# Kernel optimization log

Measured on AMD Instinct MI355X. Metric: run time of the kernel, lower is better.

## Reference

```python
import jax, jax.numpy as jnp
import numpy as np

JITTER_EPS = 0.01
TOP_K = 8


def setup_inputs() -> dict:
    key = jax.random.key(0)
    k1, k2, k3 = jax.random.split(key, 3)
    N, D, E = 16384, 4096, 64
    x = jax.random.normal(k1, (N, D), dtype=jnp.float32)
    W = jax.random.normal(k2, (D, E), dtype=jnp.float32) * (1.0 / np.sqrt(D))
    score_bias = jnp.zeros((E,), dtype=jnp.float32)
    noise = jax.random.uniform(k3, (N, D), dtype=jnp.float32)
    return {"x": x, "W": W, "score_bias": score_bias, "noise": noise}


def reference(x, W, score_bias, noise):
    E = W.shape[1]
    # jitter (training mode): x * (low + noise * (high - low))
    low = 1.0 - JITTER_EPS
    span = 2.0 * JITTER_EPS
    xj = x * (low + noise * span)
    # router logits: (N, E)
    logits = jnp.einsum("nd,de->ne", xj, W)
    scores = jax.nn.softmax(logits, axis=-1)
    # bias-corrected top-k (DeepSeek-v3 aux-loss-free balancing): indices from
    # biased scores (no grad), weights gathered from unbiased scores.
    biased = jax.lax.stop_gradient(scores) + score_bias[None, :]
    _, expert_indices = jax.lax.top_k(biased, TOP_K)  # (N, top_k) int32
    expert_weights = jnp.take_along_axis(scores, expert_indices, axis=-1)
    # L2-normalize expert weights per token
    norm = jnp.sqrt(jnp.sum(expert_weights * expert_weights, axis=-1, keepdims=True))
    expert_weights = expert_weights / norm
    # histc over expert indices -> batch size per expert
    batch_size_per_expert = jnp.bincount(expert_indices.reshape(-1), length=E)
    return (logits, scores, expert_weights, expert_indices, batch_size_per_expert)
```

## Files before the change

### kernel.cpp

```cpp
#include <hip/hip_runtime.h>
#include <math.h>


#define N_TOK 16384
#define DIM   4096
#define NEXP  64
#define TOPK  8

#define BM 64
#define BK 64
#define KSPLIT 4
#define KCHUNKS (DIM / (BK * KSPLIT))
#define XS_STRIDE 68

template<int ATOMIC_OUT>
__global__ __launch_bounds__(256, 4) void gemm_logits_kernel(
    const float* __restrict__ x, const float* __restrict__ W,
    const float* __restrict__ noise, float* __restrict__ out)
{
    __shared__ float xs[BM * XS_STRIDE];
    __shared__ float ws[BK * NEXP];

    const int t = threadIdx.x;
    const int rowBase = blockIdx.x * BM;
    const int kOff = blockIdx.y * (DIM / KSPLIT);
    const int eg = t & 15;
    const int rg = t >> 4;

    float acc[4][4];
#pragma unroll
    for (int m = 0; m < 4; ++m)
#pragma unroll
        for (int n = 0; n < 4; ++n) acc[m][n] = 0.0f;

    float4 px[4], pn[4], pw[4];

#pragma unroll
    for (int i = 0; i < 4; ++i) {
        const int f  = t + i * 256;
        const int r  = f >> 4;
        const int c4 = f & 15;
        const size_t g = (size_t)(rowBase + r) * DIM + (size_t)(kOff + c4 * 4);
        px[i] = *(const float4*)(x + g);
        pn[i] = *(const float4*)(noise + g);
        pw[i] = *(const float4*)(W + (size_t)kOff * NEXP + (size_t)f * 4);
    }

    for (int kt = 0; kt < KCHUNKS; ++kt) {
        __syncthreads();
#pragma unroll
        for (int i = 0; i < 4; ++i) {
            const int f  = t + i * 256;
            const int r  = f >> 4;
            const int c4 = f & 15;
            const float4 xv = px[i], nv = pn[i];
            float4 j;
            j.x = xv.x * (0.99f + 0.02f * nv.x);
            j.y = xv.y * (0.99f + 0.02f * nv.y);
            j.z = xv.z * (0.99f + 0.02f * nv.z);
            j.w = xv.w * (0.99f + 0.02f * nv.w);
            *(float4*)&xs[r * XS_STRIDE + c4 * 4] = j;
            *(float4*)&ws[f * 4] = pw[i];
        }
        __syncthreads();

        if (kt + 1 < KCHUNKS) {
            const int k0 = kOff + (kt + 1) * BK;
#pragma unroll
            for (int i = 0; i < 4; ++i) {
                const int f  = t + i * 256;
                const int r  = f >> 4;
                const int c4 = f & 15;
                const size_t g = (size_t)(rowBase + r) * DIM + (size_t)(k0 + c4 * 4);
                px[i] = *(const float4*)(x + g);
                pn[i] = *(const float4*)(noise + g);
                pw[i] = *(const float4*)(W + (size_t)k0 * NEXP + (size_t)f * 4);
            }
        }

        const float4* xs4 = (const float4*)xs;
        const float4* ws4 = (const float4*)ws;
#pragma unroll 4
        for (int kk4 = 0; kk4 < 16; ++kk4) {
            const float4 b0 = ws4[(kk4 * 4 + 0) * 16 + eg];
            const float4 b1 = ws4[(kk4 * 4 + 1) * 16 + eg];
            const float4 b2 = ws4[(kk4 * 4 + 2) * 16 + eg];
            const float4 b3 = ws4[(kk4 * 4 + 3) * 16 + eg];
#pragma unroll
            for (int m = 0; m < 4; ++m) {
                const float4 a = xs4[(rg * 4 + m) * 17 + kk4];
                acc[m][0] += a.x * b0.x; acc[m][1] += a.x * b0.y;
                acc[m][2] += a.x * b0.z; acc[m][3] += a.x * b0.w;
                acc[m][0] += a.y * b1.x; acc[m][1] += a.y * b1.y;
                acc[m][2] += a.y * b1.z; acc[m][3] += a.y * b1.w;
                acc[m][0] += a.z * b2.x; acc[m][1] += a.z * b2.y;
                acc[m][2] += a.z * b2.z; acc[m][3] += a.z * b2.w;
                acc[m][0] += a.w * b3.x; acc[m][1] += a.w * b3.y;
                acc[m][2] += a.w * b3.z; acc[m][3] += a.w * b3.w;
            }
        }
    }

    if (ATOMIC_OUT) {
#pragma unroll
        for (int m = 0; m < 4; ++m)
#pragma unroll
            for (int n = 0; n < 4; ++n)
                atomicAdd(out + (size_t)(rowBase + rg * 4 + m) * NEXP + eg * 4 + n,
                          acc[m][n]);
    } else {
        float* dst = out + (size_t)blockIdx.y * N_TOK * NEXP;
#pragma unroll
        for (int m = 0; m < 4; ++m) {
            float4 o;
            o.x = acc[m][0]; o.y = acc[m][1]; o.z = acc[m][2]; o.w = acc[m][3];
            *(float4*)(dst + (size_t)(rowBase + rg * 4 + m) * NEXP + eg * 4) = o;
        }
    }
}

__global__ __launch_bounds__(64, 1) void router_topk_kernel(
    const float* part, int nsplit, int writeLogits,
    const float* __restrict__ score_bias,
    float* logits, float* __restrict__ scores,
    float* __restrict__ weights, float* __restrict__ indicesF,
    float* __restrict__ histF)
{
    __shared__ float tile[64 * 65];
    __shared__ float bs[NEXP];
    __shared__ int   hist[NEXP];

    const int t = threadIdx.x;
    const int rowBase = blockIdx.x * 64;
    bs[t] = score_bias[t];
    hist[t] = 0;
    __syncthreads();

    const size_t sstride = (size_t)N_TOK * NEXP;

#pragma unroll
    for (int i = 0; i < 16; ++i) {
        const int f   = t + i * 64;
        const int row = f >> 4;
        const int c4  = f & 15;
        const size_t g = (size_t)(rowBase + row) * NEXP + (size_t)(c4 * 4);
        float4 v = *(const float4*)(part + g);
        for (int s = 1; s < nsplit; ++s) {
            const float4 p = *(const float4*)(part + (size_t)s * sstride + g);
            v.x += p.x; v.y += p.y; v.z += p.z; v.w += p.w;
        }
        if (writeLogits) *(float4*)(logits + g) = v;
        float* dst = &tile[row * 65 + c4 * 4];
        dst[0] = v.x; dst[1] = v.y; dst[2] = v.z; dst[3] = v.w;
    }
    __syncthreads();

    float a[NEXP];
#pragma unroll
    for (int j = 0; j < NEXP; ++j) a[j] = tile[t * 65 + j];

    float m0 = a[0], m1 = a[1], m2 = a[2], m3 = a[3];
#pragma unroll
    for (int j = 4; j < NEXP; j += 4) {
        m0 = fmaxf(m0, a[j + 0]); m1 = fmaxf(m1, a[j + 1]);
        m2 = fmaxf(m2, a[j + 2]); m3 = fmaxf(m3, a[j + 3]);
    }
    const float mx = fmaxf(fmaxf(m0, m1), fmaxf(m2, m3));

    float s0 = 0.f, s1 = 0.f, s2 = 0.f, s3 = 0.f;
#pragma unroll
    for (int j = 0; j < NEXP; j += 4) {
        a[j + 0] = expf(a[j + 0] - mx); s0 += a[j + 0];
        a[j + 1] = expf(a[j + 1] - mx); s1 += a[j + 1];
        a[j + 2] = expf(a[j + 2] - mx); s2 += a[j + 2];
        a[j + 3] = expf(a[j + 3] - mx); s3 += a[j + 3];
    }
    const float sinv = 1.0f / ((s0 + s1) + (s2 + s3));
#pragma unroll
    for (int j = 0; j < NEXP; ++j) a[j] *= sinv;

#pragma unroll
    for (int j = 0; j < NEXP; ++j) tile[t * 65 + j] = a[j];

#pragma unroll
    for (int j = 0; j < NEXP; ++j) a[j] += bs[j];

    float wv[TOPK]; int wi[TOPK];
    float ssq = 0.0f;
#pragma unroll
    for (int k = 0; k < TOPK; ++k) {
        float mA = a[0],  mB = a[16], mC = a[32], mD = a[48];
        int   iA = 0,     iB = 16,    iC = 32,    iD = 48;
#pragma unroll
        for (int j = 1; j < 16; ++j) {
            if (a[j]      > mA) { mA = a[j];      iA = j; }
            if (a[16 + j] > mB) { mB = a[16 + j]; iB = 16 + j; }
            if (a[32 + j] > mC) { mC = a[32 + j]; iC = 32 + j; }
            if (a[48 + j] > mD) { mD = a[48 + j]; iD = 48 + j; }
        }
        float m = mA; int mi = iA;
        if (mB > m) { m = mB; mi = iB; }
        if (mC > m) { m = mC; mi = iC; }
        if (mD > m) { m = mD; mi = iD; }

        const float w = tile[t * 65 + mi];
        wv[k] = w; wi[k] = mi; ssq += w * w;
#pragma unroll
        for (int j = 0; j < NEXP; ++j) if (j == mi) a[j] = -INFINITY;
    }

    const float rn = 1.0f / sqrtf(ssq);
    const size_t ro = (size_t)(rowBase + t) * TOPK;
#pragma unroll
    for (int k = 0; k < TOPK; ++k) {
        weights[ro + k]  = wv[k] * rn;
        indicesF[ro + k] = (float)wi[k];
        atomicAdd(&hist[wi[k]], 1);
    }
    __syncthreads();

#pragma unroll
    for (int i = 0; i < 16; ++i) {
        const int f   = t + i * 64;
        const int row = f >> 4;
        const int c4  = f & 15;
        const float* src = &tile[row * 65 + c4 * 4];
        float4 o; o.x = src[0]; o.y = src[1]; o.z = src[2]; o.w = src[3];
        *(float4*)(scores + (size_t)(rowBase + row) * NEXP + (size_t)(c4 * 4)) = o;
    }
    atomicAdd(&histF[t], (float)hist[t]);
}

extern "C" void kernel_launch(void* const* d_in, const int* in_sizes, int n_in,
                              void* d_out, int out_size, void* d_ws, size_t ws_size,
                              hipStream_t stream)
{
    const float* x     = (const float*)d_in[0];
    const float* W     = (const float*)d_in[1];
    const float* sbias = (const float*)d_in[2];
    const float* noise = (const float*)d_in[3];

    float* out      = (float*)d_out;
    float* logits   = out;
    float* scores   = out + (size_t)N_TOK * NEXP;
    float* weights  = out + 2ull * N_TOK * NEXP;
    float* indicesF = weights + (size_t)N_TOK * TOPK;
    float* histF    = indicesF + (size_t)N_TOK * TOPK;

    hipMemsetAsync(histF, 0, NEXP * sizeof(float), stream);

    const size_t partialBytes = (size_t)KSPLIT * N_TOK * NEXP * sizeof(float);
    dim3 ggrid(N_TOK / BM, KSPLIT);

    if (d_ws != nullptr && ws_size >= partialBytes) {
        float* partial = (float*)d_ws;
        gemm_logits_kernel<0><<<ggrid, 256, 0, stream>>>(x, W, noise, partial);
        router_topk_kernel<<<N_TOK / 64, 64, 0, stream>>>(
            partial, KSPLIT, 1, sbias, logits, scores, weights, indicesF, histF);
    } else {
        hipMemsetAsync(logits, 0, (size_t)N_TOK * NEXP * sizeof(float), stream);
        gemm_logits_kernel<1><<<ggrid, 256, 0, stream>>>(x, W, noise, logits);
        router_topk_kernel<<<N_TOK / 64, 64, 0, stream>>>(
            logits, 1, 0, sbias, logits, scores, weights, indicesF, histF);
    }
}
```

Before: 626.3 us.

## Double-buffer GEMM shared tiles with XOR swizzle and 2x8 thread tiles

Rewrites the jittered-logits GEMM main loop to use two shared-memory buffers with a BK of 32. This allows one barrier per chunk, with the next chunk's global loads issued before compute and staged after it. The x tile now uses an XOR swizzle instead of padding to avoid LDS bank conflicts. The per-thread tile changes from 4x4 to 2x8. These changes target barrier stalls and LDS conflicts, at the cost of more loop iterations and a changed register and LDS access pattern.

After: 580.9 us. -7.3%, faster.

```diff
diff --git a/kernel.cpp b/kernel.cpp
--- a/kernel.cpp
+++ b/kernel.cpp
@@ -8,113 +8,131 @@
 #define TOPK  8
 
 #define BM 64
-#define BK 64
+#define BK 32
 #define KSPLIT 4
-#define KCHUNKS (DIM / (BK * KSPLIT))
-#define XS_STRIDE 68
+#define KPERSPLIT (DIM / KSPLIT)
+#define NCH (KPERSPLIT / BK)
+
+#define ISSUE_LOADS(KT)                                                     \
+    {                                                                       \
+        const int k0_ = kOff + (KT) * BK;                                   \
+        _Pragma("unroll")                                                   \
+        for (int i_ = 0; i_ < 2; ++i_) {                                    \
+            const int f_ = i_ * 256 + t;                                    \
+            const int r_ = f_ >> 3;                                         \
+            const int c_ = f_ & 7;                                          \
+            const size_t g_ = (size_t)(rowBase + r_) * DIM                  \
+                            + (size_t)(k0_ + c_ * 4);                       \
+            px[i_]  = *(const float4*)(x + g_);                             \
+            pn[i_]  = *(const float4*)(noise + g_);                         \
+            pwv[i_] = *(const float4*)(W + (size_t)k0_ * NEXP               \
+                                         + (size_t)f_ * 4);                 \
+        }                                                                   \
+    }
+
+#define STAGE(B)                                                            \
+    {                                                                       \
+        _Pragma("unroll")                                                   \
+        for (int i_ = 0; i_ < 2; ++i_) {                                    \
+            const int f_ = i_ * 256 + t;                                    \
+            const int r_ = f_ >> 3;                                         \
+            const int c_ = f_ & 7;                                          \
+            const float4 xv_ = px[i_], nv_ = pn[i_];                        \
+            float4 j_;                                                      \
+            j_.x = xv_.x * (0.99f + 0.02f * nv_.x);                         \
+            j_.y = xv_.y * (0.99f + 0.02f * nv_.y);                         \
+            j_.z = xv_.z * (0.99f + 0.02f * nv_.z);                         \
+            j_.w = xv_.w * (0.99f + 0.02f * nv_.w);                         \
+            const int slot_ = r_ * 8 + (c_ ^ ((r_ >> 1) & 7));              \
+            *(float4*)&xs[B][slot_ * 4] = j_;                               \
+            *(float4*)&ws[B][f_ * 4]    = pwv[i_];                          \
+        }                                                                   \
+    }
 
 template<int ATOMIC_OUT>
 __global__ __launch_bounds__(256, 4) void gemm_logits_kernel(
     const float* __restrict__ x, const float* __restrict__ W,
     const float* __restrict__ noise, float* __restrict__ out)
 {
-    __shared__ float xs[BM * XS_STRIDE];
-    __shared__ float ws[BK * NEXP];
+    __shared__ float xs[2][BM * BK];
+    __shared__ float ws[2][BK * NEXP];
 
     const int t = threadIdx.x;
     const int rowBase = blockIdx.x * BM;
-    const int kOff = blockIdx.y * (DIM / KSPLIT);
-    const int eg = t & 15;
-    const int rg = t >> 4;
-
-    float acc[4][4];
-#pragma unroll
-    for (int m = 0; m < 4; ++m)
-#pragma unroll
-        for (int n = 0; n < 4; ++n) acc[m][n] = 0.0f;
-
-    float4 px[4], pn[4], pw[4];
-
-#pragma unroll
-    for (int i = 0; i < 4; ++i) {
-        const int f  = t + i * 256;
-        const int r  = f >> 4;
-        const int c4 = f & 15;
-        const size_t g = (size_t)(rowBase + r) * DIM + (size_t)(kOff + c4 * 4);
-        px[i] = *(const float4*)(x + g);
-        pn[i] = *(const float4*)(noise + g);
-        pw[i] = *(const float4*)(W + (size_t)kOff * NEXP + (size_t)f * 4);
-    }
-
-    for (int kt = 0; kt < KCHUNKS; ++kt) {
+    const int kOff = blockIdx.y * KPERSPLIT;
+    const int eg = t & 7;
+    const int rg = t >> 3;
+    const int eg2 = eg * 2;
+
+    float acc[2][8];
+#pragma unroll
+    for (int m = 0; m < 2; ++m)
+#pragma unroll
+        for (int n = 0; n < 8; ++n) acc[m][n] = 0.0f;
+
+    float4 px[2], pn[2], pwv[2];
+
+    ISSUE_LOADS(0)
+    STAGE(0)
+
+    for (int kt = 0; kt < NCH; ++kt) {
+        const int cb = kt & 1;
         __syncthreads();
-#pragma unroll
-        for (int i = 0; i < 4; ++i) {
-            const int f  = t + i * 256;
-            const int r  = f >> 4;
-            const int c4 = f & 15;
-            const float4 xv = px[i], nv = pn[i];
-            float4 j;
-            j.x = xv.x * (0.99f + 0.02f * nv.x);
-            j.y = xv.y * (0.99f + 0.02f * nv.y);
-            j.z = xv.z * (0.99f + 0.02f * nv.z);
-            j.w = xv.w * (0.99f + 0.02f * nv.w);
-            *(float4*)&xs[r * XS_STRIDE + c4 * 4] = j;
-            *(float4*)&ws[f * 4] = pw[i];
-        }
-        __syncthreads();
-
-        if (kt + 1 < KCHUNKS) {
-            const int k0 = kOff + (kt + 1) * BK;
-#pragma unroll
-            for (int i = 0; i < 4; ++i) {
-                const int f  = t + i * 256;
-                const int r  = f >> 4;
-                const int c4 = f & 15;
-                const size_t g = (size_t)(rowBase + r) * DIM + (size_t)(k0 + c4 * 4);
-                px[i] = *(const float4*)(x + g);
-                pn[i] = *(const float4*)(noise + g);
-                pw[i] = *(const float4*)(W + (size_t)k0 * NEXP + (size_t)f * 4);
+        if (kt + 1 < NCH) {
+            ISSUE_LOADS(kt + 1)
+        }
+
+        const float4* xs4 = (const float4*)xs[cb];
+        const float4* ws4 = (const float4*)ws[cb];
+        const int r0 = rg * 2;
+        const int sw = rg & 7;
+
+#pragma unroll
+        for (int kk4 = 0; kk4 < 8; ++kk4) {
+            const float4 a0 = xs4[(r0 + 0) * 8 + (kk4 ^ sw)];
+            const float4 a1 = xs4[(r0 + 1) * 8 + (kk4 ^ sw)];
+#define KSTEP(q, A0Q, A1Q)                                                  \
+            {                                                               \
+                const float4 b0 = ws4[(kk4 * 4 + q) * 16 + eg2];            \
+                const float4 b1 = ws4[(kk4 * 4 + q) * 16 + eg2 + 1];        \
+                acc[0][0] += A0Q * b0.x; acc[0][1] += A0Q * b0.y;           \
+                acc[0][2] += A0Q * b0.z; acc[0][3] += A0Q * b0.w;           \
+                acc[0][4] += A0Q * b1.x; acc[0][5] += A0Q * b1.y;           \
+                acc[0][6] += A0Q * b1.z; acc[0][7] += A0Q * b1.w;           \
+                acc[1][0] += A1Q * b0.x; acc[1][1] += A1Q * b0.y;           \
+                acc[1][2] += A1Q * b0.z; acc[1][3] += A1Q * b0.w;           \
+                acc[1][4] += A1Q * b1.x; acc[1][5] += A1Q * b1.y;           \
+                acc[1][6] += A1Q * b1.z; acc[1][7] += A1Q * b1.w;           \
             }
-        }
-
-        const float4* xs4 = (const float4*)xs;
-        const float4* ws4 = (const float4*)ws;
-#pragma unroll 4
-        for (int kk4 = 0; kk4 < 16; ++kk4) {
-            const float4 b0 = ws4[(kk4 * 4 + 0) * 16 + eg];
-            const float4 b1 = ws4[(kk4 * 4 + 1) * 16 + eg];
-            const float4 b2 = ws4[(kk4 * 4 + 2) * 16 + eg];
-            const float4 b3 = ws4[(kk4 * 4 + 3) * 16 + eg];
-#pragma unroll
-            for (int m = 0; m < 4; ++m) {
-                const float4 a = xs4[(rg * 4 + m) * 17 + kk4];
-                acc[m][0] += a.x * b0.x; acc[m][1] += a.x * b0.y;
-                acc[m][2] += a.x * b0.z; acc[m][3] += a.x * b0.w;
-                acc[m][0] += a.y * b1.x; acc[m][1] += a.y * b1.y;
-                acc[m][2] += a.y * b1.z; acc[m][3] += a.y * b1.w;
-                acc[m][0] += a.z * b2.x; acc[m][1] += a.z * b2.y;
-                acc[m][2] += a.z * b2.z; acc[m][3] += a.z * b2.w;
-                acc[m][0] += a.w * b3.x; acc[m][1] += a.w * b3.y;
-                acc[m][2] += a.w * b3.z; acc[m][3] += a.w * b3.w;
-            }
+            KSTEP(0, a0.x, a1.x)
+            KSTEP(1, a0.y, a1.y)
+            KSTEP(2, a0.z, a1.z)
+            KSTEP(3, a0.w, a1.w)
+#undef KSTEP
+        }
+
+        if (kt + 1 < NCH) {
+            STAGE(cb ^ 1)
         }
     }
 
     if (ATOMIC_OUT) {
 #pragma unroll
-        for (int m = 0; m < 4; ++m)
-#pragma unroll
-            for (int n = 0; n < 4; ++n)
-                atomicAdd(out + (size_t)(rowBase + rg * 4 + m) * NEXP + eg * 4 + n,
+        for (int m = 0; m < 2; ++m)
+#pragma unroll
+            for (int n = 0; n < 8; ++n)
+                atomicAdd(out + (size_t)(rowBase + rg * 2 + m) * NEXP + eg * 8 + n,
                           acc[m][n]);
     } else {
         float* dst = out + (size_t)blockIdx.y * N_TOK * NEXP;
 #pragma unroll
-        for (int m = 0; m < 4; ++m) {
-            float4 o;
-            o.x = acc[m][0]; o.y = acc[m][1]; o.z = acc[m][2]; o.w = acc[m][3];
-            *(float4*)(dst + (size_t)(rowBase + rg * 4 + m) * NEXP + eg * 4) = o;
+        for (int m = 0; m < 2; ++m) {
+            float4 o0, o1;
+            o0.x = acc[m][0]; o0.y = acc[m][1]; o0.z = acc[m][2]; o0.w = acc[m][3];
+            o1.x = acc[m][4]; o1.y = acc[m][5]; o1.z = acc[m][6]; o1.w = acc[m][7];
+            float* rowp = dst + (size_t)(rowBase + rg * 2 + m) * NEXP + eg * 8;
+            *(float4*)(rowp)     = o0;
+            *(float4*)(rowp + 4) = o1;
         }
     }
 }
```
